# Optimization experiments

Hardware: AMD Instinct MI355X
Metric: run time of the kernel (lower is better)

## Reference

```python
import jax, jax.numpy as jnp
import numpy as np

# samplelist from init_kwargs: coarse node i -> fine nodes (i, i+16)
SAMPLELIST = [[i, i + 16] for i in range(16)]
INDEX = np.array([c for grp in SAMPLELIST for c in grp])  # flattened, len 32
N_NODES = len(SAMPLELIST)   # 16 coarse nodes
KSIZE = 2                   # len of each samplelist group
BATCH, FEAT = 8192, 64      # features == dct_n == input_feature


def setup_inputs() -> dict:
    key = jax.random.key(0)
    k1, k2, k3 = jax.random.split(key, 3)
    x = jax.random.normal(k1, (BATCH, FEAT, 3, N_NODES), dtype=jnp.float32)
    # per-node nn.Linear(3, 3*KSIZE): stacked weights [N, 3k, 3], biases [N, 3k]
    bound = 1.0 / np.sqrt(3.0)
    W = jax.random.uniform(k2, (N_NODES, 3 * KSIZE, 3), jnp.float32, -bound, bound)
    b = jax.random.uniform(k3, (N_NODES, 3 * KSIZE), jnp.float32, -bound, bound)
    return {"x": x, "W": W, "b": b}


def reference(x, W, b):
    B, F, C, N = x.shape  # C == 3
    k = KSIZE
    # Fused block-diagonal matmul replacing the per-node Linear loop:
    # for node n: y_n = x[:,:,:,n] @ W_n^T + b_n  -> [B,F,3k]
    y = jnp.einsum('bfcn,noc->bfno', x, W) + b          # [B,F,N,3k]
    # torch reshape (B*F, 3k) -> (B*F, 3, k): output index o = c*k + m
    # then cat(dim=3) over nodes => last-dim order is node-major: col = n*k + m
    y = y.reshape(B, F, N, 3, k).transpose(0, 1, 3, 2, 4).reshape(B, F, 3, N * k)
    # Faithful replication of the original in-place aliased column reorder
    # (y = y1 then y[..., index[i]] = y1[..., i] sequentially on the SAME buffer).
    # N*k = 32 fixed iterations, tiny fixed loop.
    for i in range(N * k):
        y = y.at[:, :, :, int(INDEX[i])].set(y[:, :, :, i])
    return y
```

## Files before the change

kernel.cpp:

```cpp
#include <hip/hip_runtime.h>


#define BATCH 8192
#define FEAT  64
#define BF_TOTAL (BATCH * FEAT)
#define ROWS_PER_BLOCK 64
#define THREADS 256

__constant__ int c_SRC[32] = {
    0, 2, 4, 6, 8, 10, 12, 14,
    1, 5, 9, 13, 3, 11, 7, 15,
    1, 3, 5, 7, 9, 11, 13, 15,
    3, 7, 11, 15, 7, 15, 15, 31
};

__global__ __launch_bounds__(THREADS)
void GraphUpSample_12120397709982_kernel(const float* __restrict__ x,
                                         const float* __restrict__ W,
                                         const float* __restrict__ bia,
                                         float* __restrict__ out)
{
    __shared__ float xs[ROWS_PER_BLOCK * 48];

    const int tid  = threadIdx.x;
    const int fc0  = tid & 7;
    const int rset = tid >> 3;
    const long long rowbase = (long long)blockIdx.x * ROWS_PER_BLOCK;

    const float4* xg  = (const float4*)(x + rowbase * 48);
    float4*       xsv = (float4*)xs;
#pragma unroll
    for (int j = 0; j < 3; ++j)
        xsv[tid + j * THREADS] = xg[tid + j * THREADS];

    int   nn[4];
    float4 wr[3][4];
#pragma unroll
    for (int s = 0; s < 4; ++s) {
        const int src = c_SRC[fc0 * 4 + s];
        const int n   = src >> 1;
        const int m   = src & 1;
        nn[s] = n;
#pragma unroll
        for (int c = 0; c < 3; ++c) {
            const int o = 2 * c + m;
            const float* wp = W + (n * 6 + o) * 3;
            wr[c][s] = make_float4(wp[0], wp[1], wp[2], bia[n * 6 + o]);
        }
    }
    __syncthreads();

    float4* og = (float4*)(out + rowbase * 96);
#pragma unroll
    for (int rr = 0; rr < 2; ++rr) {
        const int row = rset + rr * 32;
        const float* xr = xs + row * 48;

        float xv[3][4];
#pragma unroll
        for (int cp = 0; cp < 3; ++cp)
#pragma unroll
            for (int s = 0; s < 4; ++s)
                xv[cp][s] = xr[cp * 16 + nn[s]];

#pragma unroll
        for (int c = 0; c < 3; ++c) {
            float4 o4;
            o4.x = fmaf(xv[0][0], wr[c][0].x, fmaf(xv[1][0], wr[c][0].y, fmaf(xv[2][0], wr[c][0].z, wr[c][0].w)));
            o4.y = fmaf(xv[0][1], wr[c][1].x, fmaf(xv[1][1], wr[c][1].y, fmaf(xv[2][1], wr[c][1].z, wr[c][1].w)));
            o4.z = fmaf(xv[0][2], wr[c][2].x, fmaf(xv[1][2], wr[c][2].y, fmaf(xv[2][2], wr[c][2].z, wr[c][2].w)));
            o4.w = fmaf(xv[0][3], wr[c][3].x, fmaf(xv[1][3], wr[c][3].y, fmaf(xv[2][3], wr[c][3].z, wr[c][3].w)));
            og[row * 24 + c * 8 + fc0] = o4;
        }
    }
}

extern "C" void kernel_launch(void* const* d_in, const int* in_sizes, int n_in,
                              void* d_out, int out_size, void* d_ws, size_t ws_size,
                              hipStream_t stream) {
    const float* x = (const float*)d_in[0];
    const float* W = (const float*)d_in[1];
    const float* b = (const float*)d_in[2];
    float* out = (float*)d_out;

    const int blocks = BF_TOTAL / ROWS_PER_BLOCK;
    GraphUpSample_12120397709982_kernel<<<blocks, THREADS, 0, stream>>>(x, W, b, out);
}
```

Before: 65.94 us.

## Give each wavefront its own LDS tile loop with register-prefetched next tile

Each wavefront now handles 64 rows as four 16-row tiles in a private, padded LDS region. The next tile's global loads go into registers while the current tile is computed, and the block-wide __syncthreads is dropped. The grid shrinks fourfold so each block covers 256 rows. The intent is to overlap global loads with compute and cut bank conflicts through the 52-float row stride, at the cost of fewer blocks and more registers. There is no intra-wave barrier between LDS writes and reads; it relies on lockstep execution within a 64-wide wavefront.

```diff
diff --git a/kernel.cpp b/kernel.cpp
--- a/kernel.cpp
+++ b/kernel.cpp
@@ -4,8 +4,10 @@
 #define BATCH 8192
 #define FEAT  64
 #define BF_TOTAL (BATCH * FEAT)
-#define ROWS_PER_BLOCK 64
 #define THREADS 256
+#define TILE_ROWS 16
+#define TILES 4
+#define XROWF 52
 
 __constant__ int c_SRC[32] = {
     0, 2, 4, 6, 8, 10, 12, 14,
@@ -20,20 +22,17 @@
                                          const float* __restrict__ bia,
                                          float* __restrict__ out)
 {
-    __shared__ float xs[ROWS_PER_BLOCK * 48];
+    __shared__ float xs[4 * TILE_ROWS * XROWF];
 
     const int tid  = threadIdx.x;
-    const int fc0  = tid & 7;
-    const int rset = tid >> 3;
-    const long long rowbase = (long long)blockIdx.x * ROWS_PER_BLOCK;
+    const int widx = tid >> 6;
+    const int lane = tid & 63;
+    const int fc0  = lane & 7;
+    const int rset = lane >> 3;
+    const long long wid = (long long)blockIdx.x * 4 + widx;
+    const long long rowbase = wid * 64;
 
-    const float4* xg  = (const float4*)(x + rowbase * 48);
-    float4*       xsv = (float4*)xs;
-#pragma unroll
-    for (int j = 0; j < 3; ++j)
-        xsv[tid + j * THREADS] = xg[tid + j * THREADS];
-
-    int   nn[4];
+    int    nn[4];
     float4 wr[3][4];
 #pragma unroll
     for (int s = 0; s < 4; ++s) {
@@ -43,34 +42,63 @@
         nn[s] = n;
 #pragma unroll
         for (int c = 0; c < 3; ++c) {
-            const int o = 2 * c + m;
-            const float* wp = W + (n * 6 + o) * 3;
-            wr[c][s] = make_float4(wp[0], wp[1], wp[2], bia[n * 6 + o]);
+            const float* wp = W + (n * 6 + 2 * c + m) * 3;
+            wr[c][s] = make_float4(wp[0], wp[1], wp[2], bia[n * 6 + 2 * c + m]);
         }
     }
-    __syncthreads();
 
-    float4* og = (float4*)(out + rowbase * 96);
+    float*  wlds  = xs + widx * (TILE_ROWS * XROWF);
+    float4* wlds4 = (float4*)wlds;
+    const float4* xg = (const float4*)(x + rowbase * 48);
+    float4*       og = (float4*)(out + rowbase * 96);
+
+    float4 stg[3];
 #pragma unroll
-    for (int rr = 0; rr < 2; ++rr) {
-        const int row = rset + rr * 32;
-        const float* xr = xs + row * 48;
-
-        float xv[3][4];
+    for (int i = 0; i < 3; ++i) stg[i] = xg[lane + 64 * i];
 #pragma unroll
-        for (int cp = 0; cp < 3; ++cp)
-#pragma unroll
-            for (int s = 0; s < 4; ++s)
-                xv[cp][s] = xr[cp * 16 + nn[s]];
+    for (int i = 0; i < 3; ++i) {
+        const int p = lane + 64 * i, row = p / 12, k = p - row * 12;
+        wlds4[row * 13 + k] = stg[i];
+    }
 
 #pragma unroll
-        for (int c = 0; c < 3; ++c) {
-            float4 o4;
-            o4.x = fmaf(xv[0][0], wr[c][0].x, fmaf(xv[1][0], wr[c][0].y, fmaf(xv[2][0], wr[c][0].z, wr[c][0].w)));
-            o4.y = fmaf(xv[0][1], wr[c][1].x, fmaf(xv[1][1], wr[c][1].y, fmaf(xv[2][1], wr[c][1].z, wr[c][1].w)));
-            o4.z = fmaf(xv[0][2], wr[c][2].x, fmaf(xv[1][2], wr[c][2].y, fmaf(xv[2][2], wr[c][2].z, wr[c][2].w)));
-            o4.w = fmaf(xv[0][3], wr[c][3].x, fmaf(xv[1][3], wr[c][3].y, fmaf(xv[2][3], wr[c][3].z, wr[c][3].w)));
-            og[row * 24 + c * 8 + fc0] = o4;
+    for (int t = 0; t < TILES; ++t) {
+        float4 nxt[3];
+        if (t < TILES - 1) {
+#pragma unroll
+            for (int i = 0; i < 3; ++i)
+                nxt[i] = xg[(t + 1) * 192 + lane + 64 * i];
+        }
+
+#pragma unroll
+        for (int rr = 0; rr < 2; ++rr) {
+            const int row = rset + rr * 8;
+            const float* xr = wlds + row * XROWF;
+
+            float xv[3][4];
+#pragma unroll
+            for (int cp = 0; cp < 3; ++cp)
+#pragma unroll
+                for (int s = 0; s < 4; ++s)
+                    xv[cp][s] = xr[cp * 16 + nn[s]];
+
+#pragma unroll
+            for (int c = 0; c < 3; ++c) {
+                float4 o4;
+                o4.x = fmaf(xv[0][0], wr[c][0].x, fmaf(xv[1][0], wr[c][0].y, fmaf(xv[2][0], wr[c][0].z, wr[c][0].w)));
+                o4.y = fmaf(xv[0][1], wr[c][1].x, fmaf(xv[1][1], wr[c][1].y, fmaf(xv[2][1], wr[c][1].z, wr[c][1].w)));
+                o4.z = fmaf(xv[0][2], wr[c][2].x, fmaf(xv[1][2], wr[c][2].y, fmaf(xv[2][2], wr[c][2].z, wr[c][2].w)));
+                o4.w = fmaf(xv[0][3], wr[c][3].x, fmaf(xv[1][3], wr[c][3].y, fmaf(xv[2][3], wr[c][3].z, wr[c][3].w)));
+                og[t * 384 + row * 24 + c * 8 + fc0] = o4;
+            }
+        }
+
+        if (t < TILES - 1) {
+#pragma unroll
+            for (int i = 0; i < 3; ++i) {
+                const int p = lane + 64 * i, row = p / 12, k = p - row * 12;
+                wlds4[row * 13 + k] = nxt[i];
+            }
         }
     }
 }
@@ -83,6 +111,6 @@
     const float* b = (const float*)d_in[2];
     float* out = (float*)d_out;
 
-    const int blocks = BF_TOTAL / ROWS_PER_BLOCK;
+    const int blocks = BF_TOTAL / (64 * 4);
     GraphUpSample_12120397709982_kernel<<<blocks, THREADS, 0, stream>>>(x, W, b, out);
 }
```

After: 61.70 us. -6.4%, faster.
